# Performance work log

Hardware: AMD Instinct MI355X
Metric: run time of the kernel (lower is better)

Reference implementation:

```python
import jax, jax.numpy as jnp
import numpy as np

N_HEADS = 16
HEAD_SIZE = 128  # n_embd // n_vq_heads = 2048 // 16
N_OPTIONS = 512


def setup_inputs() -> dict:
    key = jax.random.key(0)
    k1, k2, k3 = jax.random.split(key, 3)
    B, S, E = 4, 2048, N_HEADS * HEAD_SIZE
    x = jax.random.normal(k1, (B, S, E), dtype=jnp.float32)
    vq_head_weights = jax.random.normal(k2, (N_HEADS, N_OPTIONS, HEAD_SIZE), dtype=jnp.float32)
    vq_codebooks = jax.random.normal(k3, (N_HEADS, N_OPTIONS, HEAD_SIZE), dtype=jnp.float32)
    temperature = jnp.float32(1.0)
    return {
        "x": x,
        "vq_head_weights": vq_head_weights,
        "vq_codebooks": vq_codebooks,
        "temperature": temperature,
    }


def reference(x, vq_head_weights, vq_codebooks, temperature):
    # Training-mode forward of VQizer (softmax path).
    B, S, E = x.shape
    H, O, A = vq_head_weights.shape  # heads, options, head_size
    x_prepped = x.reshape(B, S, H, A)
    # per-head logits over codebook options
    logits = jnp.einsum('bsha,hoa->bsho', x_prepped, vq_head_weights)
    probs = jax.nn.softmax(logits / temperature, axis=-1)
    out = jnp.einsum('bsho,hoa->bsha', probs, vq_codebooks)
    return out.reshape(B, S, H * A)
```

## Files before the change

kernel.cpp:

```cpp
#include <hip/hip_runtime.h>
#include <math.h>

#define NHEADS 16
#define HS     128
#define NOPT   512
#define TB     128
#define OC     32
#define NCH    16
#define NITER  8
#define EMB    2048
#define LOG2E  1.44269504088896340736f
#define THRD   11.0f

typedef short bf16x8 __attribute__((ext_vector_type(8)));
typedef _Float16 f16x8 __attribute__((ext_vector_type(8)));
typedef unsigned short u16x8 __attribute__((ext_vector_type(8)));
typedef float f32x4 __attribute__((ext_vector_type(4)));
typedef float f32x16 __attribute__((ext_vector_type(16)));
typedef unsigned u32x4 __attribute__((ext_vector_type(4)));

__device__ __forceinline__ unsigned short f2bf(float f) {
    union { float f; unsigned u; } v; v.f = f;
    unsigned r = v.u + 0x7FFFu + ((v.u >> 16) & 1u);
    return (unsigned short)(r >> 16);
}
__device__ __forceinline__ float bf2f(unsigned short h) {
    union { unsigned u; float f; } v; v.u = ((unsigned)h) << 16;
    return v.f;
}
__device__ __forceinline__ unsigned short f2h(float f) {
    const _Float16 h = (_Float16)f;
    return __builtin_bit_cast(unsigned short, h);
}
__device__ __forceinline__ void gll16(const void* gptr, void* lptr) {
    __builtin_amdgcn_global_load_lds(
        (const __attribute__((address_space(1))) void*)gptr,
        (__attribute__((address_space(3))) void*)lptr,
        16, 0, 0);
}
__device__ __forceinline__ unsigned pkrtz(float lo, float hi) {
    unsigned r;
    asm("v_cvt_pkrtz_f16_f32 %0, %1, %2" : "=v"(r) : "v"(lo), "v"(hi));
    return r;
}
__device__ __forceinline__ void pl32swap(unsigned &a, unsigned &b) {
    asm volatile("v_permlane32_swap_b32 %0, %1" : "+v"(a), "+v"(b));
}
__device__ __forceinline__ f32x16 mfma32h(f16x8 a, f16x8 b, f32x16 c) {
    return __builtin_amdgcn_mfma_f32_32x32x16_f16(a, b, c, 0, 0, 0);
}

#define SUBELEMS 4096
#define WS_C0  (NHEADS * NCH * SUBELEMS)
#define WS_TOTAL_BYTES ((size_t)(WS_C0 + NHEADS * NCH * SUBELEMS) * 2)

__global__ __launch_bounds__(256) void vq_prep(const float* __restrict__ W,
                                               const float* __restrict__ C,
                                               const float* __restrict__ temp,
                                               unsigned short* __restrict__ ws)
{
    const int b = blockIdx.x, t = threadIdx.x;
    if (b < NHEADS * NCH) {
        const float scW = (1.0f / temp[0]) * LOG2E;
        const float* src = W + (size_t)b * OC * HS;
        unsigned short* dst = ws + (size_t)b * SUBELEMS;
        for (int k4 = 0; k4 < 16; ++k4) {
            const int e = k4 * 256 + t;
            const int opt = e >> 7, k = e & 127;
            const int kb = k >> 4, hf = (k >> 3) & 1, j = k & 7;
            const int l = hf * 32 + opt;
            dst[kb * 512 + l * 8 + j] = f2h(src[e] * scW);
        }
    } else {
        const int b2 = b - NHEADS * NCH;
        const float* src = C + (size_t)b2 * OC * HS;
        unsigned short* dst = ws + WS_C0 + (size_t)b2 * SUBELEMS;
        for (int k4 = 0; k4 < 16; ++k4) {
            const int e = k4 * 256 + t;
            const int opt = e >> 7, a = e & 127;
            const int q = opt >> 4, hf = (opt >> 3) & 1, j = opt & 7;
            const int nt = a >> 5, l = hf * 32 + (a & 31);
            dst[(nt * 2 + q) * 512 + l * 8 + j] = f2h(src[e]);
        }
    }
}

__global__ __launch_bounds__(256, 2) void vq_main(
    const float* __restrict__ x, const unsigned short* __restrict__ ws,
    float* __restrict__ out)
{
    __shared__ unsigned short wbuf[2][2 * SUBELEMS];
    __shared__ unsigned short cbuf[2][2 * SUBELEMS];

    const int t = threadIdx.x, l = t & 63, w = t >> 6;
    const int la = l & 31, hf = l >> 5;
    const int b = blockIdx.x;
    const int head = ((b & 7) << 1) | ((b >> 3) & 1);
    const int n0 = (b >> 4) * TB;

    const char* gwbase = (const char*)(ws + (size_t)(head * NCH) * SUBELEMS);
    const char* gcbase = (const char*)(ws + WS_C0 + (size_t)(head * NCH) * SUBELEMS);
    const int l8 = l * 8;

    {
        const char* gw = gwbase + w * 4096 + l * 16;
        char* lw = (char*)&wbuf[0][0] + w * 4096;
        const char* gc = gcbase + w * 4096 + l * 16;
        char* lc = (char*)&cbuf[0][0] + w * 4096;
        #pragma unroll
        for (int i = 0; i < 4; ++i) { gll16(gw + i * 1024, lw + i * 1024);
                                      gll16(gc + i * 1024, lc + i * 1024); }
    }

    f16x8 xf[8];
    {
        const float* xr = x + (size_t)(n0 + w * 32 + la) * EMB + head * HS + hf * 8;
        #pragma unroll
        for (int kb = 0; kb < 8; ++kb) {
            const float4 v0 = *(const float4*)(xr + kb * 16);
            const float4 v1 = *(const float4*)(xr + kb * 16 + 4);
            const float vv[8] = {v0.x, v0.y, v0.z, v0.w, v1.x, v1.y, v1.z, v1.w};
            u16x8 hh;
            #pragma unroll
            for (int j = 0; j < 8; ++j) hh[j] = f2h(vv[j]);
            xf[kb] = __builtin_bit_cast(f16x8, hh);
        }
    }

    f32x16 O0 = (f32x16)0.0f, O1 = (f32x16)0.0f, O2 = (f32x16)0.0f, O3 = (f32x16)0.0f;
    float M = -1.0e30f, sacc = 0.0f;

    asm volatile("s_waitcnt vmcnt(0)" ::: "memory");
    __builtin_amdgcn_s_barrier();

    for (int cc = 0; cc < NITER; ++cc) {
        const int cur = cc & 1;
        if (cc + 1 < NITER) {
            const char* gw = gwbase + (size_t)(cc + 1) * 16384 + w * 4096 + l * 16;
            char* lw = (char*)&wbuf[cur ^ 1][0] + w * 4096;
            const char* gc = gcbase + (size_t)(cc + 1) * 16384 + w * 4096 + l * 16;
            char* lc = (char*)&cbuf[cur ^ 1][0] + w * 4096;
            #pragma unroll
            for (int i = 0; i < 4; ++i) { gll16(gw + i * 1024, lw + i * 1024);
                                          gll16(gc + i * 1024, lc + i * 1024); }
        }

        f32x16 s0a = (f32x16)0.0f, s0b = (f32x16)0.0f;
        f32x16 s1a = (f32x16)0.0f, s1b = (f32x16)0.0f;
        const unsigned short* wb0 = &wbuf[cur][0];
        const unsigned short* wb1 = &wbuf[cur][SUBELEMS];
        __builtin_amdgcn_s_setprio(1);
        #pragma unroll
        for (int kb = 0; kb < 8; ++kb) {
            const f16x8 w0 = *(const f16x8*)&wb0[kb * 512 + l8];
            const f16x8 w1 = *(const f16x8*)&wb1[kb * 512 + l8];
            if (kb & 1) { s0b = mfma32h(w0, xf[kb], s0b); s1b = mfma32h(w1, xf[kb], s1b); }
            else        { s0a = mfma32h(w0, xf[kb], s0a); s1a = mfma32h(w1, xf[kb], s1a); }
        }
        __builtin_amdgcn_s_setprio(0);
        f32x16 S0 = s0a + s0b;
        f32x16 S1 = s1a + s1b;

        float cmax = fmaxf(S0[0], S1[0]);
        #pragma unroll
        for (int i = 1; i < 16; ++i) cmax = fmaxf(fmaxf(cmax, S0[i]), S1[i]);
        cmax = fmaxf(cmax, __shfl_xor(cmax, 32));
        if (__any(cmax > M + THRD)) {
            const float Mn = fmaxf(M, cmax);
            const float fr = exp2f(M - Mn);
            M = Mn;
            sacc *= fr;
            #pragma unroll
            for (int q = 0; q < 16; ++q) {
                const int row = (q & 3) + 8 * (q >> 2) + 4 * hf;
                const float f = __shfl(fr, row);
                O0[q] *= f; O1[q] *= f; O2[q] *= f; O3[q] *= f;
            }
        }
        #pragma unroll
        for (int q = 0; q < 16; ++q) { S0[q] = exp2f(S0[q] - M); S1[q] = exp2f(S1[q] - M); }
        {
            float s8[8];
            #pragma unroll
            for (int i = 0; i < 8; ++i)
                s8[i] = (S0[2 * i] + S0[2 * i + 1]) + (S1[2 * i] + S1[2 * i + 1]);
            sacc += ((s8[0] + s8[1]) + (s8[2] + s8[3])) +
                    ((s8[4] + s8[5]) + (s8[6] + s8[7]));
        }

        unsigned pk0 = pkrtz(S0[0],  S0[1]),  pk1 = pkrtz(S0[2],  S0[3]);
        unsigned pk2 = pkrtz(S0[4],  S0[5]),  pk3 = pkrtz(S0[6],  S0[7]);
        unsigned pk4 = pkrtz(S0[8],  S0[9]),  pk5 = pkrtz(S0[10], S0[11]);
        unsigned pk6 = pkrtz(S0[12], S0[13]), pk7 = pkrtz(S0[14], S0[15]);
        pl32swap(pk0, pk2); pl32swap(pk1, pk3);
        pl32swap(pk4, pk6); pl32swap(pk5, pk7);
        const f16x8 pa0 = __builtin_bit_cast(f16x8, (u32x4){pk0, pk1, pk2, pk3});
        const f16x8 pa1 = __builtin_bit_cast(f16x8, (u32x4){pk4, pk5, pk6, pk7});
        unsigned qk0 = pkrtz(S1[0],  S1[1]),  qk1 = pkrtz(S1[2],  S1[3]);
        unsigned qk2 = pkrtz(S1[4],  S1[5]),  qk3 = pkrtz(S1[6],  S1[7]);
        unsigned qk4 = pkrtz(S1[8],  S1[9]),  qk5 = pkrtz(S1[10], S1[11]);
        unsigned qk6 = pkrtz(S1[12], S1[13]), qk7 = pkrtz(S1[14], S1[15]);
        pl32swap(qk0, qk2); pl32swap(qk1, qk3);
        pl32swap(qk4, qk6); pl32swap(qk5, qk7);
        const f16x8 pa2 = __builtin_bit_cast(f16x8, (u32x4){qk0, qk1, qk2, qk3});
        const f16x8 pa3 = __builtin_bit_cast(f16x8, (u32x4){qk4, qk5, qk6, qk7});

        const unsigned short* cb0 = &cbuf[cur][0];
        const unsigned short* cb1 = &cbuf[cur][SUBELEMS];
        __builtin_amdgcn_s_setprio(1);
        #pragma unroll
        for (int nt = 0; nt < 4; ++nt) {
            f32x16& O = (nt == 0) ? O0 : (nt == 1) ? O1 : (nt == 2) ? O2 : O3;
            O = mfma32h(pa0, *(const f16x8*)&cb0[(nt * 2 + 0) * 512 + l8], O);
            O = mfma32h(pa1, *(const f16x8*)&cb0[(nt * 2 + 1) * 512 + l8], O);
            O = mfma32h(pa2, *(const f16x8*)&cb1[(nt * 2 + 0) * 512 + l8], O);
            O = mfma32h(pa3, *(const f16x8*)&cb1[(nt * 2 + 1) * 512 + l8], O);
        }
        __builtin_amdgcn_s_setprio(0);

        asm volatile("s_waitcnt vmcnt(0)" ::: "memory");
        if (cc + 1 < NITER) __builtin_amdgcn_s_barrier();
    }

    const float stot = sacc + __shfl_xor(sacc, 32);
    const float rs = 1.0f / stot;
    #pragma unroll
    for (int q = 0; q < 16; ++q) {
        const int row = (q & 3) + 8 * (q >> 2) + 4 * hf;
        const float rq = __shfl(rs, row);
        float* op = out + (size_t)(n0 + w * 32 + row) * EMB + head * HS + la;
        op[0]  = O0[q] * rq;
        op[32] = O1[q] * rq;
        op[64] = O2[q] * rq;
        op[96] = O3[q] * rq;
    }
}

__global__ __launch_bounds__(256, 2) void vq_fwd_mfma(
    const float* __restrict__ x, const float* __restrict__ W,
    const float* __restrict__ C, const float* __restrict__ temp,
    float* __restrict__ out)
{
    __shared__ unsigned short xh_lds[64 * HS];
    __shared__ unsigned short xl_lds[64 * HS];
    __shared__ unsigned short wst[2][64 * HS];
    __shared__ unsigned short p_lds[4][16 * 64];

    const int t = threadIdx.x, l = t & 63, w = t >> 6, lr = l & 15, lk = l >> 4;
    const int b = blockIdx.x;
    const int h = ((b & 7) << 1) | ((b >> 3) & 1);
    const int n0 = (b >> 4) * 64;
    const float invT = 1.0f / temp[0];

    #pragma unroll
    for (int kk = 0; kk < 4; ++kk) {
        const int g = t + 256 * kk;
        const int row = g >> 4, c8 = (g & 15) * 8;
        const float* src = x + (size_t)(n0 + row) * EMB + h * HS + c8;
        const float4 v0 = *(const float4*)src;
        const float4 v1 = *(const float4*)(src + 4);
        float vv[8] = {v0.x, v0.y, v0.z, v0.w, v1.x, v1.y, v1.z, v1.w};
        u16x8 hh, ll;
        #pragma unroll
        for (int j = 0; j < 8; ++j) {
            const unsigned short hb = f2bf(vv[j]);
            hh[j] = hb; ll[j] = f2bf(vv[j] - bf2f(hb));
        }
        const int idx = row * HS + (c8 ^ ((row & 7) << 3));
        *(u16x8*)&xh_lds[idx] = hh;
        *(u16x8*)&xl_lds[idx] = ll;
    }

    f32x4 acc[32];
    #pragma unroll
    for (int i = 0; i < 32; ++i) acc[i] = f32x4{0.f, 0.f, 0.f, 0.f};
    bf16x8 axh[4], axl[4];

    #pragma unroll
    for (int c = 0; c < 8; ++c) {
        if (c) __syncthreads();
        #pragma unroll
        for (int kk = 0; kk < 4; ++kk) {
            const int g = t + 256 * kk;
            const int row = g >> 4, c8 = (g & 15) * 8;
            const float* src = W + ((size_t)h * NOPT + c * 64 + row) * HS + c8;
            const float4 v0 = *(const float4*)src;
            const float4 v1 = *(const float4*)(src + 4);
            float vv[8] = {v0.x, v0.y, v0.z, v0.w, v1.x, v1.y, v1.z, v1.w};
            u16x8 hh, ll;
            #pragma unroll
            for (int j = 0; j < 8; ++j) {
                const unsigned short hb = f2bf(vv[j]);
                hh[j] = hb; ll[j] = f2bf(vv[j] - bf2f(hb));
            }
            const int idx = row * HS + (c8 ^ ((row & 7) << 3));
            *(u16x8*)&wst[0][idx] = hh;
            *(u16x8*)&wst[1][idx] = ll;
        }
        __syncthreads();
        if (c == 0) {
            const int arow = w * 16 + lr;
            #pragma unroll
            for (int ks = 0; ks < 4; ++ks) {
                const int ai = arow * HS + ((lk * 8 + ks * 32) ^ ((arow & 7) << 3));
                axh[ks] = *(const bf16x8*)&xh_lds[ai];
                axl[ks] = *(const bf16x8*)&xl_lds[ai];
            }
        }
        #pragma unroll
        for (int nt = 0; nt < 4; ++nt) {
            const int brow = nt * 16 + lr;
            #pragma unroll
            for (int ks = 0; ks < 4; ++ks) {
                const int bi = brow * HS + ((lk * 8 + ks * 32) ^ ((brow & 7) << 3));
                const bf16x8 bh = *(const bf16x8*)&wst[0][bi];
                const bf16x8 bl = *(const bf16x8*)&wst[1][bi];
                acc[c*4+nt] = __builtin_amdgcn_mfma_f32_16x16x32_bf16(axh[ks], bh, acc[c*4+nt], 0, 0, 0);
                acc[c*4+nt] = __builtin_amdgcn_mfma_f32_16x16x32_bf16(axl[ks], bh, acc[c*4+nt], 0, 0, 0);
                acc[c*4+nt] = __builtin_amdgcn_mfma_f32_16x16x32_bf16(axh[ks], bl, acc[c*4+nt], 0, 0, 0);
            }
        }
    }

    float mx[4], rsn[4];
    #pragma unroll
    for (int r = 0; r < 4; ++r) {
        float m = -3.0e38f;
        #pragma unroll
        for (int i = 0; i < 32; ++i) m = fmaxf(m, acc[i][r]);
        m *= invT;
        #pragma unroll
        for (int s = 1; s < 16; s <<= 1) m = fmaxf(m, __shfl_xor(m, s));
        float sum = 0.f;
        #pragma unroll
        for (int i = 0; i < 32; ++i) sum += exp2f((acc[i][r] * invT - m) * LOG2E);
        #pragma unroll
        for (int s = 1; s < 16; s <<= 1) sum += __shfl_xor(sum, s);
        mx[r] = m; rsn[r] = 1.0f / sum;
    }

    f32x4 oacc[8];
    #pragma unroll
    for (int i = 0; i < 8; ++i) oacc[i] = f32x4{0.f, 0.f, 0.f, 0.f};
    const int pr_ = t & 31, ag = t >> 5;
    #pragma unroll
    for (int c = 0; c < 8; ++c) {
        __syncthreads();
        {
            const float* c0p = C + ((size_t)h * NOPT + c * 64 + 2 * pr_) * HS + ag * 16;
            float va[16], vb[16];
            #pragma unroll
            for (int q = 0; q < 4; ++q) {
                const float4 u0 = ((const float4*)c0p)[q];
                const float4 u1 = ((const float4*)(c0p + HS))[q];
                va[q*4+0] = u0.x; va[q*4+1] = u0.y; va[q*4+2] = u0.z; va[q*4+3] = u0.w;
                vb[q*4+0] = u1.x; vb[q*4+1] = u1.y; vb[q*4+2] = u1.z; vb[q*4+3] = u1.w;
            }
            unsigned* ct32 = (unsigned*)&wst[0][0];
            #pragma unroll
            for (int j = 0; j < 16; ++j) {
                const int a = ag * 16 + j;
                const unsigned pkv = (unsigned)f2bf(va[j]) | ((unsigned)f2bf(vb[j]) << 16);
                ct32[a * 32 + (pr_ ^ ((a & 7) << 2))] = pkv;
            }
        }
        #pragma unroll
        for (int nt = 0; nt < 4; ++nt) {
            #pragma unroll
            for (int r = 0; r < 4; ++r) {
                const float p = exp2f((acc[c*4+nt][r] * invT - mx[r]) * LOG2E);
                const int prow = lk * 4 + r;
                const int pcol = nt * 16 + lr;
                p_lds[w][prow * 64 + (pcol ^ ((prow & 7) << 3))] = f2bf(p);
            }
        }
        __syncthreads();
        #pragma unroll
        for (int ks = 0; ks < 2; ++ks) {
            const int ai = lr * 64 + ((lk * 8 + ks * 32) ^ ((lr & 7) << 3));
            const bf16x8 pa = *(const bf16x8*)&p_lds[w][ai];
            #pragma unroll
            for (int nt = 0; nt < 8; ++nt) {
                const int brow = nt * 16 + lr;
                const int bi = brow * 64 + ((lk * 8 + ks * 32) ^ ((brow & 7) << 3));
                const bf16x8 cbv = *(const bf16x8*)&wst[0][bi];
                oacc[nt] = __builtin_amdgcn_mfma_f32_16x16x32_bf16(pa, cbv, oacc[nt], 0, 0, 0);
            }
        }
    }

    #pragma unroll
    for (int nt = 0; nt < 8; ++nt) {
        #pragma unroll
        for (int r = 0; r < 4; ++r) {
            const int tok = n0 + w * 16 + lk * 4 + r;
            out[(size_t)tok * EMB + h * HS + nt * 16 + lr] = oacc[nt][r] * rsn[r];
        }
    }
}

extern "C" void kernel_launch(void* const* d_in, const int* in_sizes, int n_in,
                              void* d_out, int out_size, void* d_ws, size_t ws_size,
                              hipStream_t stream) {
    const float* x = (const float*)d_in[0];
    const float* W = (const float*)d_in[1];
    const float* C = (const float*)d_in[2];
    const float* T = (const float*)d_in[3];
    float* out     = (float*)d_out;

    const int ntok = in_sizes[0] / EMB;

    if (ws_size >= WS_TOTAL_BYTES) {
        hipLaunchKernelGGL(vq_prep, dim3(NHEADS * NCH * 2), dim3(256), 0, stream,
                           W, C, T, (unsigned short*)d_ws);
        const int nblk = (ntok / TB) * NHEADS;
        hipLaunchKernelGGL(vq_main, dim3(nblk), dim3(256), 0, stream,
                           x, (const unsigned short*)d_ws, out);
    } else {
        const int nblk = (ntok / 64) * NHEADS;
        hipLaunchKernelGGL(vq_fwd_mfma, dim3(nblk), dim3(256), 0, stream,
                           x, W, C, T, out);
    }
}
```

Measured before the change: 72.54 us.

## Process one 32-option chunk per iteration and vectorize prep layout stores

The main loop now handles one 32-option codebook chunk per iteration (16 iterations instead of 8), which halves the LDS double-buffer footprint and the per-iteration register state (one score tile instead of two). The goal is lower LDS and register pressure and possibly better occupancy. The cost is twice as many barriers, online-softmax max checks and rescales. The prep kernel is also rewritten so each thread writes a full 16-byte packed vector instead of scattered 2-byte stores.

New measurement: 71.48 us, median of 3. No clear change (-1.5%).

```diff
diff --git a/kernel.cpp b/kernel.cpp
--- a/kernel.cpp
+++ b/kernel.cpp
@@ -7,7 +7,7 @@
 #define TB     128
 #define OC     32
 #define NCH    16
-#define NITER  8
+#define NITER  16
 #define EMB    2048
 #define LOG2E  1.44269504088896340736f
 #define THRD   11.0f
@@ -64,23 +64,35 @@
         const float scW = (1.0f / temp[0]) * LOG2E;
         const float* src = W + (size_t)b * OC * HS;
         unsigned short* dst = ws + (size_t)b * SUBELEMS;
-        for (int k4 = 0; k4 < 16; ++k4) {
-            const int e = k4 * 256 + t;
-            const int opt = e >> 7, k = e & 127;
-            const int kb = k >> 4, hf = (k >> 3) & 1, j = k & 7;
-            const int l = hf * 32 + opt;
-            dst[kb * 512 + l * 8 + j] = f2h(src[e] * scW);
+        #pragma unroll
+        for (int i = 0; i < 2; ++i) {
+            const int pid = i * 256 + t;
+            const int kb = pid >> 6, l = pid & 63;
+            const int base = (l & 31) * 128 + kb * 16 + (l >> 5) * 8;
+            const float4 v0 = *(const float4*)(src + base);
+            const float4 v1 = *(const float4*)(src + base + 4);
+            u16x8 hh;
+            hh[0] = f2h(v0.x * scW); hh[1] = f2h(v0.y * scW);
+            hh[2] = f2h(v0.z * scW); hh[3] = f2h(v0.w * scW);
+            hh[4] = f2h(v1.x * scW); hh[5] = f2h(v1.y * scW);
+            hh[6] = f2h(v1.z * scW); hh[7] = f2h(v1.w * scW);
+            *(u16x8*)&dst[kb * 512 + l * 8] = hh;
         }
     } else {
         const int b2 = b - NHEADS * NCH;
         const float* src = C + (size_t)b2 * OC * HS;
         unsigned short* dst = ws + WS_C0 + (size_t)b2 * SUBELEMS;
-        for (int k4 = 0; k4 < 16; ++k4) {
-            const int e = k4 * 256 + t;
-            const int opt = e >> 7, a = e & 127;
-            const int q = opt >> 4, hf = (opt >> 3) & 1, j = opt & 7;
-            const int nt = a >> 5, l = hf * 32 + (a & 31);
-            dst[(nt * 2 + q) * 512 + l * 8 + j] = f2h(src[e]);
+        #pragma unroll
+        for (int i = 0; i < 2; ++i) {
+            const int pid = i * 256 + t;
+            const int ntq = pid >> 6, l = pid & 63;
+            const int nt = ntq >> 1, q = ntq & 1;
+            const int a = nt * 32 + (l & 31);
+            const int o0 = q * 16 + (l >> 5) * 8;
+            u16x8 hh;
+            #pragma unroll
+            for (int j = 0; j < 8; ++j) hh[j] = f2h(src[(o0 + j) * 128 + a]);
+            *(u16x8*)&dst[ntq * 512 + l * 8] = hh;
         }
     }
 }
@@ -89,8 +101,8 @@
     const float* __restrict__ x, const unsigned short* __restrict__ ws,
     float* __restrict__ out)
 {
-    __shared__ unsigned short wbuf[2][2 * SUBELEMS];
-    __shared__ unsigned short cbuf[2][2 * SUBELEMS];
+    __shared__ unsigned short wbuf[2][SUBELEMS];
+    __shared__ unsigned short cbuf[2][SUBELEMS];
 
     const int t = threadIdx.x, l = t & 63, w = t >> 6;
     const int la = l & 31, hf = l >> 5;
@@ -103,13 +115,12 @@
     const int l8 = l * 8;
 
     {
-        const char* gw = gwbase + w * 4096 + l * 16;
-        char* lw = (char*)&wbuf[0][0] + w * 4096;
-        const char* gc = gcbase + w * 4096 + l * 16;
-        char* lc = (char*)&cbuf[0][0] + w * 4096;
-        #pragma unroll
-        for (int i = 0; i < 4; ++i) { gll16(gw + i * 1024, lw + i * 1024);
-                                      gll16(gc + i * 1024, lc + i * 1024); }
+        const char* gw = gwbase + w * 2048 + l * 16;
+        char* lw = (char*)&wbuf[0][0] + w * 2048;
+        const char* gc = gcbase + w * 2048 + l * 16;
+        char* lc = (char*)&cbuf[0][0] + w * 2048;
+        gll16(gw, lw); gll16(gw + 1024, lw + 1024);
+        gll16(gc, lc); gll16(gc + 1024, lc + 1024);
     }
 
     f16x8 xf[8];
@@ -136,34 +147,25 @@
     for (int cc = 0; cc < NITER; ++cc) {
         const int cur = cc & 1;
         if (cc + 1 < NITER) {
-            const char* gw = gwbase + (size_t)(cc + 1) * 16384 + w * 4096 + l * 16;
-            char* lw = (char*)&wbuf[cur ^ 1][0] + w * 4096;
-            const char* gc = gcbase + (size_t)(cc + 1) * 16384 + w * 4096 + l * 16;
-            char* lc = (char*)&cbuf[cur ^ 1][0] + w * 4096;
-            #pragma unroll
-            for (int i = 0; i < 4; ++i) { gll16(gw + i * 1024, lw + i * 1024);
-                                          gll16(gc + i * 1024, lc + i * 1024); }
-        }
-
-        f32x16 s0a = (f32x16)0.0f, s0b = (f32x16)0.0f;
-        f32x16 s1a = (f32x16)0.0f, s1b = (f32x16)0.0f;
-        const unsigned short* wb0 = &wbuf[cur][0];
-        const unsigned short* wb1 = &wbuf[cur][SUBELEMS];
+            const char* gw = gwbase + (size_t)(cc + 1) * 8192 + w * 2048 + l * 16;
+            char* lw = (char*)&wbuf[cur ^ 1][0] + w * 2048;
+            const char* gc = gcbase + (size_t)(cc + 1) * 8192 + w * 2048 + l * 16;
+            char* lc = (char*)&cbuf[cur ^ 1][0] + w * 2048;
+            gll16(gw, lw); gll16(gw + 1024, lw + 1024);
+            gll16(gc, lc); gll16(gc + 1024, lc + 1024);
+        }
+
+        f32x16 S = (f32x16)0.0f;
+        const unsigned short* wb = &wbuf[cur][0];
         __builtin_amdgcn_s_setprio(1);
         #pragma unroll
-        for (int kb = 0; kb < 8; ++kb) {
-            const f16x8 w0 = *(const f16x8*)&wb0[kb * 512 + l8];
-            const f16x8 w1 = *(const f16x8*)&wb1[kb * 512 + l8];
-            if (kb & 1) { s0b = mfma32h(w0, xf[kb], s0b); s1b = mfma32h(w1, xf[kb], s1b); }
-            else        { s0a = mfma32h(w0, xf[kb], s0a); s1a = mfma32h(w1, xf[kb], s1a); }
-        }
+        for (int kb = 0; kb < 8; ++kb)
+            S = mfma32h(*(const f16x8*)&wb[kb * 512 + l8], xf[kb], S);
         __builtin_amdgcn_s_setprio(0);
-        f32x16 S0 = s0a + s0b;
-        f32x16 S1 = s1a + s1b;
-
-        float cmax = fmaxf(S0[0], S1[0]);
-        #pragma unroll
-        for (int i = 1; i < 16; ++i) cmax = fmaxf(fmaxf(cmax, S0[i]), S1[i]);
+
+        float cmax = fmaxf(S[0], S[1]);
+        #pragma unroll
+        for (int i = 2; i < 16; i += 2) cmax = fmaxf(fmaxf(cmax, S[i]), S[i + 1]);
         cmax = fmaxf(cmax, __shfl_xor(cmax, 32));
         if (__any(cmax > M + THRD)) {
             const float Mn = fmaxf(M, cmax);
@@ -178,43 +180,31 @@
             }
         }
         #pragma unroll
-        for (int q = 0; q < 16; ++q) { S0[q] = exp2f(S0[q] - M); S1[q] = exp2f(S1[q] - M); }
+        for (int q = 0; q < 16; ++q) S[q] = exp2f(S[q] - M);
         {
             float s8[8];
             #pragma unroll
-            for (int i = 0; i < 8; ++i)
-                s8[i] = (S0[2 * i] + S0[2 * i + 1]) + (S1[2 * i] + S1[2 * i + 1]);
+            for (int i = 0; i < 8; ++i) s8[i] = S[2 * i] + S[2 * i + 1];
             sacc += ((s8[0] + s8[1]) + (s8[2] + s8[3])) +
                     ((s8[4] + s8[5]) + (s8[6] + s8[7]));
         }
 
-        unsigned pk0 = pkrtz(S0[0],  S0[1]),  pk1 = pkrtz(S0[2],  S0[3]);
-        unsigned pk2 = pkrtz(S0[4],  S0[5]),  pk3 = pkrtz(S0[6],  S0[7]);
-        unsigned pk4 = pkrtz(S0[8],  S0[9]),  pk5 = pkrtz(S0[10], S0[11]);
-        unsigned pk6 = pkrtz(S0[12], S0[13]), pk7 = pkrtz(S0[14], S0[15]);
+        unsigned pk0 = pkrtz(S[0],  S[1]),  pk1 = pkrtz(S[2],  S[3]);
+        unsigned pk2 = pkrtz(S[4],  S[5]),  pk3 = pkrtz(S[6],  S[7]);
+        unsigned pk4 = pkrtz(S[8],  S[9]),  pk5 = pkrtz(S[10], S[11]);
+        unsigned pk6 = pkrtz(S[12], S[13]), pk7 = pkrtz(S[14], S[15]);
         pl32swap(pk0, pk2); pl32swap(pk1, pk3);
         pl32swap(pk4, pk6); pl32swap(pk5, pk7);
         const f16x8 pa0 = __builtin_bit_cast(f16x8, (u32x4){pk0, pk1, pk2, pk3});
         const f16x8 pa1 = __builtin_bit_cast(f16x8, (u32x4){pk4, pk5, pk6, pk7});
-        unsigned qk0 = pkrtz(S1[0],  S1[1]),  qk1 = pkrtz(S1[2],  S1[3]);
-        unsigned qk2 = pkrtz(S1[4],  S1[5]),  qk3 = pkrtz(S1[6],  S1[7]);
-        unsigned qk4 = pkrtz(S1[8],  S1[9]),  qk5 = pkrtz(S1[10], S1[11]);
-        unsigned qk6 = pkrtz(S1[12], S1[13]), qk7 = pkrtz(S1[14], S1[15]);
-        pl32swap(qk0, qk2); pl32swap(qk1, qk3);
-        pl32swap(qk4, qk6); pl32swap(qk5, qk7);
-        const f16x8 pa2 = __builtin_bit_cast(f16x8, (u32x4){qk0, qk1, qk2, qk3});
-        const f16x8 pa3 = __builtin_bit_cast(f16x8, (u32x4){qk4, qk5, qk6, qk7});
-
-        const unsigned short* cb0 = &cbuf[cur][0];
-        const unsigned short* cb1 = &cbuf[cur][SUBELEMS];
+
+        const unsigned short* cb = &cbuf[cur][0];
         __builtin_amdgcn_s_setprio(1);
         #pragma unroll
         for (int nt = 0; nt < 4; ++nt) {
             f32x16& O = (nt == 0) ? O0 : (nt == 1) ? O1 : (nt == 2) ? O2 : O3;
-            O = mfma32h(pa0, *(const f16x8*)&cb0[(nt * 2 + 0) * 512 + l8], O);
-            O = mfma32h(pa1, *(const f16x8*)&cb0[(nt * 2 + 1) * 512 + l8], O);
-            O = mfma32h(pa2, *(const f16x8*)&cb1[(nt * 2 + 0) * 512 + l8], O);
-            O = mfma32h(pa3, *(const f16x8*)&cb1[(nt * 2 + 1) * 512 + l8], O);
+            O = mfma32h(pa0, *(const f16x8*)&cb[(nt * 2 + 0) * 512 + l8], O);
+            O = mfma32h(pa1, *(const f16x8*)&cb[(nt * 2 + 1) * 512 + l8], O);
         }
         __builtin_amdgcn_s_setprio(0);
 
```
